# Optimization experiments

Hardware: AMD Instinct MI355X
Metric: run time of the kernel (lower is better)

Reference implementation:

```python
import jax, jax.numpy as jnp
import numpy as np

N_NODES = 100000
N_EDGES = 1600000
N_GRAPHS = 512
F_IN = 20
HID = 128
OUT = HID // 2


def _glorot(key, shape):
    fan_in, fan_out = shape[0], shape[1]
    lim = float(np.sqrt(6.0 / (fan_in + fan_out)))
    return jax.random.uniform(key, shape, jnp.float32, -lim, lim)


def setup_inputs() -> dict:
    key = jax.random.key(0)
    ks = jax.random.split(key, 12)
    x = jax.random.normal(ks[0], (N_NODES, F_IN), jnp.float32)
    edge_index = jax.random.randint(ks[1], (2, N_EDGES), 0, N_NODES, dtype=jnp.int64)
    batch = jnp.sort(jax.random.randint(ks[2], (N_NODES,), 0, N_GRAPHS, dtype=jnp.int64))
    return {
        "x": x,
        "edge_index": edge_index,
        "batch": batch,
        "W1": _glorot(ks[3], (F_IN, HID)), "b1": jnp.zeros((HID,), jnp.float32),
        "W2": _glorot(ks[4], (HID, HID)), "b2": jnp.zeros((HID,), jnp.float32),
        "W3": _glorot(ks[5], (HID, HID)), "b3": jnp.zeros((HID,), jnp.float32),
        "Wout": _glorot(ks[6], (HID, OUT)), "bout": jnp.zeros((OUT,), jnp.float32),
    }


def _gcn_conv(x, W, b, src, dst, num_nodes):
    # PyG GCNConv: x' = D^{-1/2} (A + I) D^{-1/2} X W + b (self-loops already in src/dst)
    xw = x @ W                                                  # [N, H]
    ones = jnp.ones(src.shape[0], dtype=xw.dtype)
    deg = jax.ops.segment_sum(ones, dst, num_segments=num_nodes)
    dinv = jnp.where(deg > 0, jax.lax.rsqrt(deg), 0.0)          # [N]
    norm = dinv[src] * dinv[dst]                                # [E+N]
    msg = xw[src] * norm[:, None]                               # gather + scale
    return jax.ops.segment_sum(msg, dst, num_segments=num_nodes) + b


def reference(x, edge_index, batch, W1, b1, W2, b2, W3, b3, Wout, bout):
    num_nodes = x.shape[0]
    loops = jnp.arange(num_nodes, dtype=edge_index.dtype)
    src = jnp.concatenate([edge_index[0], loops])
    dst = jnp.concatenate([edge_index[1], loops])

    h = jax.nn.relu(_gcn_conv(x, W1, b1, src, dst, num_nodes))
    h = jax.nn.relu(_gcn_conv(h, W2, b2, src, dst, num_nodes))
    h = jax.nn.relu(_gcn_conv(h, W3, b3, src, dst, num_nodes))

    # global_mean_pool over graph ids
    sums = jax.ops.segment_sum(h, batch, num_segments=N_GRAPHS)
    counts = jax.ops.segment_sum(jnp.ones(num_nodes, h.dtype), batch, num_segments=N_GRAPHS)
    pooled = sums / jnp.maximum(counts, 1.0)[:, None]           # [G, H]
    return pooled @ Wout + bout                                 # [G, H//2]
```

## Files before the change

### kernel.cpp

```cpp
#include <hip/hip_runtime.h>
#include <hip/hip_fp16.h>

#define N_NODES 100000
#define N_EDGES 1600000
#define N_GRAPHS 512
#define F_IN 20
#define HID 128
#define OUT_F 64

#define BUCKETS 512
#define SPAN 196
#define BCAP 3500
#define EPB 4096

typedef _Float16 half8_t __attribute__((ext_vector_type(8)));
typedef float f32x4_t __attribute__((ext_vector_type(4)));
typedef unsigned int uv4 __attribute__((ext_vector_type(4)));

__device__ inline float4 h4_to_f4(uint2 u) {
    __half2 h0 = *(__half2*)&u.x;
    __half2 h1 = *(__half2*)&u.y;
    float2 f0 = __half22float2(h0);
    float2 f1 = __half22float2(h1);
    return make_float4(f0.x, f0.y, f1.x, f1.y);
}

__device__ inline float4 f4_from(unsigned a, unsigned b) {
    __half2 h0 = *(__half2*)&a;
    __half2 h1 = *(__half2*)&b;
    float2 f0 = __half22float2(h0);
    float2 f1 = __half22float2(h1);
    return make_float4(f0.x, f0.y, f1.x, f1.y);
}

__global__ __launch_bounds__(512) void partition(const int* __restrict__ src,
                                                 const int* __restrict__ dst,
                                                 int* __restrict__ bpairs,
                                                 int* cur512) {
    __shared__ int lcnt[8][BUCKETS];
    __shared__ int woff[8][BUCKETS];
    int t = threadIdx.x;
    int wv = t >> 6;
    for (int i = t; i < 8 * BUCKETS; i += 512) ((int*)lcnt)[i] = 0;
    __syncthreads();
    int base = blockIdx.x * EPB;
    int myb[8], myp[8], myr[8];
#pragma unroll
    for (int i = 0; i < 8; ++i) {
        int e = base + i * 512 + t;
        int b = -1, p = 0, rk = 0;
        if (e < N_EDGES) {
            int s = src[e], d = dst[e];
            b = d / SPAN;
            p = (s << 9) | (d - b * SPAN);
            rk = atomicAdd(&lcnt[wv][b], 1);
        }
        myb[i] = b; myp[i] = p; myr[i] = rk;
    }
    __syncthreads();
    {
        int c[8], tot = 0;
#pragma unroll
        for (int w = 0; w < 8; ++w) { c[w] = lcnt[w][t]; tot += c[w]; }
        int gb = atomicAdd(&cur512[t], tot);
#pragma unroll
        for (int w = 0; w < 8; ++w) { woff[w][t] = gb; gb += c[w]; }
    }
    __syncthreads();
#pragma unroll
    for (int i = 0; i < 8; ++i) {
        int b = myb[i];
        if (b >= 0) {
            int p = woff[wv][b] + myr[i];
            if (p < BCAP) bpairs[(size_t)b * BCAP + p] = myp[i];
        }
    }
}

__global__ __launch_bounds__(512) void csr_build(const int* __restrict__ bpairs,
                                                 const int* __restrict__ cur512,
                                                 int* __restrict__ row_st,
                                                 int* __restrict__ csr,
                                                 const float* __restrict__ x,
                                                 __half* __restrict__ Xs) {
    __shared__ int ocnt[SPAN];
    __shared__ int sc[512];
    __shared__ int cur[SPAN];
    __shared__ int sbase;
    int b = blockIdx.x, t = threadIdx.x;

    int myc = cur512[t];
    sc[t] = myc;
    __syncthreads();
    for (int o = 1; o < BUCKETS; o <<= 1) {
        int v = (t >= o) ? sc[t - o] : 0;
        __syncthreads();
        sc[t] += v;
        __syncthreads();
    }
    if (t == b) sbase = sc[t] - myc;
    if (b == BUCKETS - 1 && t == 0) row_st[N_NODES] = N_EDGES;

    int n0 = b * SPAN;
    int span = N_NODES - n0; if (span > SPAN) span = SPAN;
    if (span < 0) span = 0;
    if (t < SPAN) ocnt[t] = 0;
    __syncthreads();

    int n = cur512[b];
    if (n > BCAP) n = BCAP;
    const int* p = bpairs + (size_t)b * BCAP;
    for (int i = t; i < n; i += 512) atomicAdd(&ocnt[p[i] & 511], 1);
    __syncthreads();
    sc[t] = (t < span) ? ocnt[t] : 0;
    __syncthreads();
    for (int o = 1; o < 512; o <<= 1) {
        int v = (t >= o) ? sc[t - o] : 0;
        __syncthreads();
        sc[t] += v;
        __syncthreads();
    }
    int base = sbase;
    if (t < span) {
        int start = sc[t] - ocnt[t];
        row_st[n0 + t] = base + start;
        cur[t] = start;
    }
    __syncthreads();
    for (int i = t; i < n; i += 512) {
        int e = p[i];
        int lp = atomicAdd(&cur[e & 511], 1);
        csr[base + lp] = e >> 9;
    }
    for (int i = t; i < span * 32; i += 512) {
        int nl = i >> 5, f = i & 31;
        float v = (f < F_IN) ? x[(size_t)(n0 + nl) * F_IN + f] : 0.f;
        float di = rsqrtf((float)(ocnt[nl] + 1));
        Xs[(size_t)(n0 + nl) * 32 + f] = __float2half(di * v);
    }
}

__global__ __launch_bounds__(256) void layer1(const __half* __restrict__ Xs,
                                              const int* __restrict__ row_st,
                                              const int* __restrict__ csr,
                                              const float* __restrict__ W,
                                              const float* __restrict__ bias,
                                              __half* __restrict__ H) {
    __shared__ float Wlds[F_IN * HID];
    __shared__ float Alds[64][F_IN];
    const int t = threadIdx.x;
    const int node0 = blockIdx.x * 64;

    for (int i = t; i < F_IN * HID; i += 256) Wlds[i] = W[i];

    const int grp = t >> 2;
    const int l   = t & 3;
    const int n   = node0 + grp;
    if (n < N_NODES) {
        int r0 = row_st[n], r1 = row_st[n + 1];
        const uv4* X4 = (const uv4*)Xs;
        uv4 u = X4[(size_t)n * 4 + l];
        float4 accL = f4_from(u[0], u[1]);
        float4 accH = f4_from(u[2], u[3]);
        int r = r0;
        for (; r + 7 < r1; r += 8) {
            int s0 = csr[r],     s1 = csr[r + 1], s2 = csr[r + 2], s3 = csr[r + 3];
            int s4 = csr[r + 4], s5 = csr[r + 5], s6 = csr[r + 6], s7 = csr[r + 7];
            uv4 vv0 = X4[(size_t)s0 * 4 + l];
            uv4 vv1 = X4[(size_t)s1 * 4 + l];
            uv4 vv2 = X4[(size_t)s2 * 4 + l];
            uv4 vv3 = X4[(size_t)s3 * 4 + l];
            uv4 vv4 = X4[(size_t)s4 * 4 + l];
            uv4 vv5 = X4[(size_t)s5 * 4 + l];
            uv4 vv6 = X4[(size_t)s6 * 4 + l];
            uv4 vv7 = X4[(size_t)s7 * 4 + l];
            uv4 vv[8] = {vv0, vv1, vv2, vv3, vv4, vv5, vv6, vv7};
#pragma unroll
            for (int j = 0; j < 8; ++j) {
                float4 aL = f4_from(vv[j][0], vv[j][1]);
                float4 aH = f4_from(vv[j][2], vv[j][3]);
                accL.x += aL.x; accL.y += aL.y; accL.z += aL.z; accL.w += aL.w;
                accH.x += aH.x; accH.y += aH.y; accH.z += aH.z; accH.w += aH.w;
            }
        }
        for (; r < r1; ++r) {
            uv4 v = X4[(size_t)csr[r] * 4 + l];
            float4 aL = f4_from(v[0], v[1]);
            float4 aH = f4_from(v[2], v[3]);
            accL.x += aL.x; accL.y += aL.y; accL.z += aL.z; accL.w += aL.w;
            accH.x += aH.x; accH.y += aH.y; accH.z += aH.z; accH.w += aH.w;
        }
        float di = rsqrtf((float)(r1 - r0 + 1));
        if (l < 2) {
            int f0 = l * 8;
            Alds[grp][f0 + 0] = di * accL.x;
            Alds[grp][f0 + 1] = di * accL.y;
            Alds[grp][f0 + 2] = di * accL.z;
            Alds[grp][f0 + 3] = di * accL.w;
            Alds[grp][f0 + 4] = di * accH.x;
            Alds[grp][f0 + 5] = di * accH.y;
            Alds[grp][f0 + 6] = di * accH.z;
            Alds[grp][f0 + 7] = di * accH.w;
        } else if (l == 2) {
            Alds[grp][16] = di * accL.x;
            Alds[grp][17] = di * accL.y;
            Alds[grp][18] = di * accL.z;
            Alds[grp][19] = di * accL.w;
        }
    }
    __syncthreads();

    const int nl = t >> 2;
    const int cb = (t & 3) * 4;
    float4 acc[8];
#pragma unroll
    for (int j = 0; j < 8; ++j) acc[j] = *(const float4*)&bias[cb + 16 * j];
#pragma unroll
    for (int k = 0; k < F_IN; ++k) {
        float a = Alds[nl][k];
        const float* Wr = &Wlds[k * HID + cb];
#pragma unroll
        for (int j = 0; j < 8; ++j) {
            float4 w = *(const float4*)&Wr[16 * j];
            acc[j].x = fmaf(a, w.x, acc[j].x);
            acc[j].y = fmaf(a, w.y, acc[j].y);
            acc[j].z = fmaf(a, w.z, acc[j].z);
            acc[j].w = fmaf(a, w.w, acc[j].w);
        }
    }
    if (node0 + nl < N_NODES) {
#pragma unroll
        for (int j = 0; j < 8; ++j) {
            int c = cb + 16 * j;
            int slice = c >> 6;
            int wi = (t & 3) + 4 * (j & 3);
            __half2 h0 = __floats2half2_rn(acc[j].x, acc[j].y);
            __half2 h1 = __floats2half2_rn(acc[j].z, acc[j].w);
            uint2 u; u.x = *(unsigned*)&h0; u.y = *(unsigned*)&h1;
            ((uint2*)H)[((size_t)slice * N_NODES + node0 + nl) * 16 + wi] = u;
        }
    }
}

__global__ __launch_bounds__(256) void gemm_mfma(const __half* __restrict__ H,
                                                 const float* __restrict__ W,
                                                 const int* __restrict__ row_st,
                                                 __half* __restrict__ T) {
    __shared__ _Float16 Whi[64 * 128];
    __shared__ _Float16 Wlo[64 * 128];
    const int t = threadIdx.x;
    const int c0 = (blockIdx.x & 1) * 64;

    for (int i = t; i < 128 * 64; i += 256) {
        int k = i >> 6, c = i & 63;
        float w = W[k * HID + c0 + c];
        _Float16 hi = (_Float16)w;
        _Float16 lo = (_Float16)((w - (float)hi) * 2048.0f);
        int addr = c * 128 + (((k >> 3) ^ (c & 15)) << 3) + (k & 7);
        Whi[addr] = hi;
        Wlo[addr] = lo;
    }
    __syncthreads();

    const int wv = t >> 6;
    const int l  = t & 63;
    const int lr = l & 15;
    const int lq = l >> 4;

    for (int rep = 0; rep < 4; ++rep) {
        int strip = ((blockIdx.x >> 1) * 4 + wv) * 4 + rep;
        if (strip >= N_NODES / 16) continue;
        int n0 = strip * 16;

        f32x4_t acc[4], acl[4];
#pragma unroll
        for (int ct = 0; ct < 4; ++ct) { acc[ct] = (f32x4_t){0,0,0,0}; acl[ct] = (f32x4_t){0,0,0,0}; }

#pragma unroll
        for (int kc = 0; kc < 4; ++kc) {
            half8_t a = *(const half8_t*)(H + ((size_t)(kc >> 1) * N_NODES + n0 + lr) * 64
                                            + (kc & 1) * 32 + lq * 8);
#pragma unroll
            for (int j = 0; j < 8; ++j) a[j] = a[j] > (_Float16)0 ? a[j] : (_Float16)0;
            int g = kc * 4 + lq;
#pragma unroll
            for (int ct = 0; ct < 4; ++ct) {
                int c = ct * 16 + lr;
                int addr = c * 128 + ((g ^ lr) << 3);
                half8_t bh = *(const half8_t*)&Whi[addr];
                half8_t bl = *(const half8_t*)&Wlo[addr];
                acc[ct] = __builtin_amdgcn_mfma_f32_16x16x32_f16(a, bh, acc[ct], 0, 0, 0);
                acl[ct] = __builtin_amdgcn_mfma_f32_16x16x32_f16(a, bl, acl[ct], 0, 0, 0);
            }
        }

        int r0 = n0 + lq * 4;
#pragma unroll
        for (int r = 0; r < 4; ++r) {
            int row = r0 + r;
            float d = rsqrtf((float)(row_st[row + 1] - row_st[row] + 1));
#pragma unroll
            for (int ct = 0; ct < 4; ++ct) {
                float v = (acc[ct][r] + acl[ct][r] * 4.8828125e-4f) * d;
                int c = c0 + ct * 16 + lr;
                T[((size_t)(c >> 6) * N_NODES + row) * 64 + (c & 63)] = __float2half(v);
            }
        }
    }
}

__global__ __launch_bounds__(256) void gather_half(const __half* __restrict__ T,
                                                   const int* __restrict__ row_st,
                                                   const int* __restrict__ csr,
                                                   const float* __restrict__ bias,
                                                   __half* __restrict__ B) {
    int t = threadIdx.x;
    int b = blockIdx.x;
    int x = b & 7;
    int slice = x >> 2;
    int chunk = (b >> 3) * 4 + (x & 3);
    int n = chunk * 32 + (t >> 3);
    int l = t & 7;
    if (n >= N_NODES) return;
    int r0 = row_st[n], r1 = row_st[n + 1];
    float di = rsqrtf((float)(r1 - r0 + 1));
    const uv4* Tf = (const uv4*)T + (size_t)slice * N_NODES * 8;
    uv4 u = Tf[(size_t)n * 8 + l];
    float4 accL = f4_from(u[0], u[1]);
    float4 accH = f4_from(u[2], u[3]);
    int r = r0;
    for (; r + 7 < r1; r += 8) {
        int s0 = csr[r],     s1 = csr[r + 1], s2 = csr[r + 2], s3 = csr[r + 3];
        int s4 = csr[r + 4], s5 = csr[r + 5], s6 = csr[r + 6], s7 = csr[r + 7];
        uv4 vv0 = Tf[(size_t)s0 * 8 + l];
        uv4 vv1 = Tf[(size_t)s1 * 8 + l];
        uv4 vv2 = Tf[(size_t)s2 * 8 + l];
        uv4 vv3 = Tf[(size_t)s3 * 8 + l];
        uv4 vv4 = Tf[(size_t)s4 * 8 + l];
        uv4 vv5 = Tf[(size_t)s5 * 8 + l];
        uv4 vv6 = Tf[(size_t)s6 * 8 + l];
        uv4 vv7 = Tf[(size_t)s7 * 8 + l];
        uv4 vv[8] = {vv0, vv1, vv2, vv3, vv4, vv5, vv6, vv7};
#pragma unroll
        for (int j = 0; j < 8; ++j) {
            float4 aL = f4_from(vv[j][0], vv[j][1]);
            float4 aH = f4_from(vv[j][2], vv[j][3]);
            accL.x += aL.x; accL.y += aL.y; accL.z += aL.z; accL.w += aL.w;
            accH.x += aH.x; accH.y += aH.y; accH.z += aH.z; accH.w += aH.w;
        }
    }
    for (; r + 3 < r1; r += 4) {
        int s0 = csr[r], s1 = csr[r + 1], s2 = csr[r + 2], s3 = csr[r + 3];
        uv4 vv0 = Tf[(size_t)s0 * 8 + l];
        uv4 vv1 = Tf[(size_t)s1 * 8 + l];
        uv4 vv2 = Tf[(size_t)s2 * 8 + l];
        uv4 vv3 = Tf[(size_t)s3 * 8 + l];
        uv4 vv[4] = {vv0, vv1, vv2, vv3};
#pragma unroll
        for (int j = 0; j < 4; ++j) {
            float4 aL = f4_from(vv[j][0], vv[j][1]);
            float4 aH = f4_from(vv[j][2], vv[j][3]);
            accL.x += aL.x; accL.y += aL.y; accL.z += aL.z; accL.w += aL.w;
            accH.x += aH.x; accH.y += aH.y; accH.z += aH.z; accH.w += aH.w;
        }
    }
    for (; r < r1; ++r) {
        uv4 v = Tf[(size_t)csr[r] * 8 + l];
        float4 aL = f4_from(v[0], v[1]);
        float4 aH = f4_from(v[2], v[3]);
        accL.x += aL.x; accL.y += aL.y; accL.z += aL.z; accL.w += aL.w;
        accH.x += aH.x; accH.y += aH.y; accH.z += aH.z; accH.w += aH.w;
    }
    const float4* bb = (const float4*)bias + slice * 16 + l * 2;
    float4 b0 = bb[0], b1 = bb[1];
    __half2 h0 = __floats2half2_rn(fmaf(di, accL.x, b0.x), fmaf(di, accL.y, b0.y));
    __half2 h1 = __floats2half2_rn(fmaf(di, accL.z, b0.z), fmaf(di, accL.w, b0.w));
    __half2 h2 = __floats2half2_rn(fmaf(di, accH.x, b1.x), fmaf(di, accH.y, b1.y));
    __half2 h3 = __floats2half2_rn(fmaf(di, accH.z, b1.z), fmaf(di, accH.w, b1.w));
    uv4 o;
    o[0] = *(unsigned*)&h0; o[1] = *(unsigned*)&h1;
    o[2] = *(unsigned*)&h2; o[3] = *(unsigned*)&h3;
    uv4* dstp = (uv4*)B + ((size_t)slice * N_NODES + n) * 8 + l;
    __builtin_nontemporal_store(o, dstp);
}

__global__ __launch_bounds__(256) void pool_head(const __half* __restrict__ H,
                                                 const int* __restrict__ batch,
                                                 const float* __restrict__ Wout,
                                                 const float* __restrict__ bout,
                                                 float* __restrict__ out) {
    __shared__ float4 part[8][32];
    __shared__ float p[HID];
    __shared__ int bounds[2];
    int g = blockIdx.x;
    int t = threadIdx.x;
    if (t < 2) {
        int target = g + t;
        int lo = 0, hi = N_NODES;
        while (lo < hi) {
            int mid = (lo + hi) >> 1;
            if (batch[mid] < target) lo = mid + 1; else hi = mid;
        }
        bounds[t] = lo;
    }
    __syncthreads();
    int lo = bounds[0], hi = bounds[1];
    int grp = t >> 5, l = t & 31;
    const uint2* Hf = (const uint2*)H;
    float4 acc = make_float4(0.f, 0.f, 0.f, 0.f);
    const size_t sbase = (size_t)(l >> 4) * N_NODES;
    const int wi = l & 15;
    for (int n = lo + grp; n < hi; n += 8) {
        float4 v = h4_to_f4(Hf[(sbase + n) * 16 + wi]);
        acc.x += fmaxf(v.x, 0.f);
        acc.y += fmaxf(v.y, 0.f);
        acc.z += fmaxf(v.z, 0.f);
        acc.w += fmaxf(v.w, 0.f);
    }
    part[grp][l] = acc;
    __syncthreads();
    if (t < 32) {
        float4 s = part[0][t];
#pragma unroll
        for (int j = 1; j < 8; ++j) {
            float4 v = part[j][t];
            s.x += v.x; s.y += v.y; s.z += v.z; s.w += v.w;
        }
        float inv = 1.0f / fmaxf((float)(hi - lo), 1.0f);
        p[t * 4 + 0] = s.x * inv;
        p[t * 4 + 1] = s.y * inv;
        p[t * 4 + 2] = s.z * inv;
        p[t * 4 + 3] = s.w * inv;
    }
    __syncthreads();
    if (t < OUT_F) {
        float acc2 = 0.f;
#pragma unroll 8
        for (int k = 0; k < HID; ++k)
            acc2 = fmaf(p[k], Wout[k * OUT_F + t], acc2);
        out[g * OUT_F + t] = acc2 + bout[t];
    }
}

extern "C" void kernel_launch(void* const* d_in, const int* in_sizes, int n_in,
                              void* d_out, int out_size, void* d_ws, size_t ws_size,
                              hipStream_t stream) {
    const float* x     = (const float*)d_in[0];
    const int*   ei    = (const int*)d_in[1];
    const int*   batch = (const int*)d_in[2];
    const float* W1    = (const float*)d_in[3];
    const float* b1    = (const float*)d_in[4];
    const float* W2    = (const float*)d_in[5];
    const float* b2    = (const float*)d_in[6];
    const float* W3    = (const float*)d_in[7];
    const float* b3    = (const float*)d_in[8];
    const float* Wout  = (const float*)d_in[9];
    const float* bout  = (const float*)d_in[10];
    float* out = (float*)d_out;

    const int* src = ei;
    const int* dst = ei + N_EDGES;

    float* A      = (float*)d_ws;
    float* Breg   = A + (size_t)N_NODES * HID;
    int*   row_st = (int*)(Breg + (size_t)N_NODES * HID);
    int*   cur512 = row_st + N_NODES + 1;
    int*   csr    = cur512 + BUCKETS;

    int*    bpairs = (int*)A;
    __half* Xs     = (__half*)((char*)A + 7168000);
    __half* T      = (__half*)A;
    __half* H      = (__half*)Breg;

    hipMemsetAsync(cur512, 0, BUCKETS * sizeof(int), stream);
    partition<<<(N_EDGES + EPB - 1) / EPB, 512, 0, stream>>>(src, dst, bpairs, cur512);
    csr_build<<<BUCKETS, 512, 0, stream>>>(bpairs, cur512, row_st, csr, x, Xs);

    layer1<<<(N_NODES + 63) / 64, 256, 0, stream>>>(Xs, row_st, csr, W1, b1, H);

    gemm_mfma<<<782, 256, 0, stream>>>(H, W2, row_st, T);
    gather_half<<<6256, 256, 0, stream>>>(T, row_st, csr, b2, H);
    gemm_mfma<<<782, 256, 0, stream>>>(H, W3, row_st, T);
    gather_half<<<6256, 256, 0, stream>>>(T, row_st, csr, b3, H);

    pool_head<<<N_GRAPHS, 256, 0, stream>>>(H, batch, Wout, bout, out);
}
```

Baseline: 343.3 us.

## Fuse aggregation and MFMA GEMM per layer, aggregate before transform

Replaces the separate transform-then-gather kernels for layers 2 and 3 with one fused kernel. It first aggregates 128-wide pre-scaled fp16 neighbour features into LDS, then multiplies by W using split hi/lo fp16 MFMA, applying bias, ReLU and the next layer's degree scaling in the epilogue. The weight hi/lo split moves into a separate prep kernel, and the activation layout changes from two 64-column slices to row-major 128. This removes the intermediate T round trip and two launches, at the cost of gathering 256-byte rows instead of 128-byte slices and a per-block weight load from global memory.

```diff
diff --git a/kernel.cpp b/kernel.cpp
--- a/kernel.cpp
+++ b/kernel.cpp
@@ -31,6 +31,13 @@
     float2 f0 = __half22float2(h0);
     float2 f1 = __half22float2(h1);
     return make_float4(f0.x, f0.y, f1.x, f1.y);
+}
+
+__device__ inline void acc8(float4& aL, float4& aH, uv4 v) {
+    float4 l_ = f4_from(v[0], v[1]);
+    float4 h_ = f4_from(v[2], v[3]);
+    aL.x += l_.x; aL.y += l_.y; aL.z += l_.z; aL.w += l_.w;
+    aH.x += h_.x; aH.y += h_.y; aH.z += h_.z; aH.w += h_.w;
 }
 
 __global__ __launch_bounds__(512) void partition(const int* __restrict__ src,
@@ -140,6 +147,21 @@
     }
 }
 
+__global__ __launch_bounds__(256) void w_prep(const float* __restrict__ W2,
+                                              const float* __restrict__ W3,
+                                              _Float16* __restrict__ Whl) {
+    int idx = blockIdx.x * 256 + threadIdx.x;
+    if (idx >= 2 * HID * HID) return;
+    int layer = idx >> 14;
+    int c = (idx >> 7) & 127;
+    int k = idx & 127;
+    float w = (layer ? W3 : W2)[k * HID + c];
+    _Float16 hi = (_Float16)w;
+    _Float16 lo = (_Float16)((w - (float)hi) * 2048.0f);
+    Whl[((size_t)layer * 2 + 0) * 16384 + c * 128 + k] = hi;
+    Whl[((size_t)layer * 2 + 1) * 16384 + c * 128 + k] = lo;
+}
+
 __global__ __launch_bounds__(256) void layer1(const __half* __restrict__ Xs,
                                               const int* __restrict__ row_st,
                                               const int* __restrict__ csr,
@@ -148,6 +170,7 @@
                                               __half* __restrict__ H) {
     __shared__ float Wlds[F_IN * HID];
     __shared__ float Alds[64][F_IN];
+    __shared__ float d1[64];
     const int t = threadIdx.x;
     const int node0 = blockIdx.x * 64;
 
@@ -156,6 +179,7 @@
     const int grp = t >> 2;
     const int l   = t & 3;
     const int n   = node0 + grp;
+    float di = 0.f;
     if (n < N_NODES) {
         int r0 = row_st[n], r1 = row_st[n + 1];
         const uv4* X4 = (const uv4*)Xs;
@@ -176,21 +200,10 @@
             uv4 vv7 = X4[(size_t)s7 * 4 + l];
             uv4 vv[8] = {vv0, vv1, vv2, vv3, vv4, vv5, vv6, vv7};
 #pragma unroll
-            for (int j = 0; j < 8; ++j) {
-                float4 aL = f4_from(vv[j][0], vv[j][1]);
-                float4 aH = f4_from(vv[j][2], vv[j][3]);
-                accL.x += aL.x; accL.y += aL.y; accL.z += aL.z; accL.w += aL.w;
-                accH.x += aH.x; accH.y += aH.y; accH.z += aH.z; accH.w += aH.w;
-            }
-        }
-        for (; r < r1; ++r) {
-            uv4 v = X4[(size_t)csr[r] * 4 + l];
-            float4 aL = f4_from(v[0], v[1]);
-            float4 aH = f4_from(v[2], v[3]);
-            accL.x += aL.x; accL.y += aL.y; accL.z += aL.z; accL.w += aL.w;
-            accH.x += aH.x; accH.y += aH.y; accH.z += aH.z; accH.w += aH.w;
-        }
-        float di = rsqrtf((float)(r1 - r0 + 1));
+            for (int j = 0; j < 8; ++j) acc8(accL, accH, vv[j]);
+        }
+        for (; r < r1; ++r) acc8(accL, accH, X4[(size_t)csr[r] * 4 + l]);
+        di = rsqrtf((float)(r1 - r0 + 1));
         if (l < 2) {
             int f0 = l * 8;
             Alds[grp][f0 + 0] = di * accL.x;
@@ -208,6 +221,7 @@
             Alds[grp][19] = di * accL.w;
         }
     }
+    if (l == 0) d1[grp] = di;
     __syncthreads();
 
     const int nl = t >> 2;
@@ -229,159 +243,134 @@
         }
     }
     if (node0 + nl < N_NODES) {
+        float dd = d1[nl];
 #pragma unroll
         for (int j = 0; j < 8; ++j) {
-            int c = cb + 16 * j;
-            int slice = c >> 6;
-            int wi = (t & 3) + 4 * (j & 3);
-            __half2 h0 = __floats2half2_rn(acc[j].x, acc[j].y);
-            __half2 h1 = __floats2half2_rn(acc[j].z, acc[j].w);
+            float vx = fmaxf(acc[j].x, 0.f) * dd;
+            float vy = fmaxf(acc[j].y, 0.f) * dd;
+            float vz = fmaxf(acc[j].z, 0.f) * dd;
+            float vw = fmaxf(acc[j].w, 0.f) * dd;
+            __half2 h0 = __floats2half2_rn(vx, vy);
+            __half2 h1 = __floats2half2_rn(vz, vw);
             uint2 u; u.x = *(unsigned*)&h0; u.y = *(unsigned*)&h1;
-            ((uint2*)H)[((size_t)slice * N_NODES + node0 + nl) * 16 + wi] = u;
-        }
-    }
-}
-
-__global__ __launch_bounds__(256) void gemm_mfma(const __half* __restrict__ H,
-                                                 const float* __restrict__ W,
-                                                 const int* __restrict__ row_st,
-                                                 __half* __restrict__ T) {
-    __shared__ _Float16 Whi[64 * 128];
-    __shared__ _Float16 Wlo[64 * 128];
-    const int t = threadIdx.x;
-    const int c0 = (blockIdx.x & 1) * 64;
-
-    for (int i = t; i < 128 * 64; i += 256) {
-        int k = i >> 6, c = i & 63;
-        float w = W[k * HID + c0 + c];
-        _Float16 hi = (_Float16)w;
-        _Float16 lo = (_Float16)((w - (float)hi) * 2048.0f);
-        int addr = c * 128 + (((k >> 3) ^ (c & 15)) << 3) + (k & 7);
-        Whi[addr] = hi;
-        Wlo[addr] = lo;
-    }
-    __syncthreads();
-
-    const int wv = t >> 6;
-    const int l  = t & 63;
-    const int lr = l & 15;
-    const int lq = l >> 4;
-
-    for (int rep = 0; rep < 4; ++rep) {
-        int strip = ((blockIdx.x >> 1) * 4 + wv) * 4 + rep;
-        if (strip >= N_NODES / 16) continue;
-        int n0 = strip * 16;
-
-        f32x4_t acc[4], acl[4];
-#pragma unroll
-        for (int ct = 0; ct < 4; ++ct) { acc[ct] = (f32x4_t){0,0,0,0}; acl[ct] = (f32x4_t){0,0,0,0}; }
-
-#pragma unroll
-        for (int kc = 0; kc < 4; ++kc) {
-            half8_t a = *(const half8_t*)(H + ((size_t)(kc >> 1) * N_NODES + n0 + lr) * 64
-                                            + (kc & 1) * 32 + lq * 8);
-#pragma unroll
-            for (int j = 0; j < 8; ++j) a[j] = a[j] > (_Float16)0 ? a[j] : (_Float16)0;
-            int g = kc * 4 + lq;
-#pragma unroll
-            for (int ct = 0; ct < 4; ++ct) {
-                int c = ct * 16 + lr;
-                int addr = c * 128 + ((g ^ lr) << 3);
-                half8_t bh = *(const half8_t*)&Whi[addr];
-                half8_t bl = *(const half8_t*)&Wlo[addr];
-                acc[ct] = __builtin_amdgcn_mfma_f32_16x16x32_f16(a, bh, acc[ct], 0, 0, 0);
-                acl[ct] = __builtin_amdgcn_mfma_f32_16x16x32_f16(a, bl, acl[ct], 0, 0, 0);
-            }
-        }
-
-        int r0 = n0 + lq * 4;
-#pragma unroll
-        for (int r = 0; r < 4; ++r) {
-            int row = r0 + r;
-            float d = rsqrtf((float)(row_st[row + 1] - row_st[row] + 1));
-#pragma unroll
-            for (int ct = 0; ct < 4; ++ct) {
-                float v = (acc[ct][r] + acl[ct][r] * 4.8828125e-4f) * d;
-                int c = c0 + ct * 16 + lr;
-                T[((size_t)(c >> 6) * N_NODES + row) * 64 + (c & 63)] = __float2half(v);
-            }
-        }
-    }
-}
-
-__global__ __launch_bounds__(256) void gather_half(const __half* __restrict__ T,
+            ((uint2*)H)[(size_t)(node0 + nl) * 32 + (t & 3) + 4 * j] = u;
+        }
+    }
+}
+
+template<int APPLY_D>
+__global__ __launch_bounds__(512) void layer_fused(const __half* __restrict__ P,
                                                    const int* __restrict__ row_st,
                                                    const int* __restrict__ csr,
+                                                   const _Float16* __restrict__ Wb,
                                                    const float* __restrict__ bias,
-                                                   __half* __restrict__ B) {
-    int t = threadIdx.x;
-    int b = blockIdx.x;
-    int x = b & 7;
-    int slice = x >> 2;
-    int chunk = (b >> 3) * 4 + (x & 3);
-    int n = chunk * 32 + (t >> 3);
-    int l = t & 7;
-    if (n >= N_NODES) return;
-    int r0 = row_st[n], r1 = row_st[n + 1];
-    float di = rsqrtf((float)(r1 - r0 + 1));
-    const uv4* Tf = (const uv4*)T + (size_t)slice * N_NODES * 8;
-    uv4 u = Tf[(size_t)n * 8 + l];
-    float4 accL = f4_from(u[0], u[1]);
-    float4 accH = f4_from(u[2], u[3]);
-    int r = r0;
-    for (; r + 7 < r1; r += 8) {
-        int s0 = csr[r],     s1 = csr[r + 1], s2 = csr[r + 2], s3 = csr[r + 3];
-        int s4 = csr[r + 4], s5 = csr[r + 5], s6 = csr[r + 6], s7 = csr[r + 7];
-        uv4 vv0 = Tf[(size_t)s0 * 8 + l];
-        uv4 vv1 = Tf[(size_t)s1 * 8 + l];
-        uv4 vv2 = Tf[(size_t)s2 * 8 + l];
-        uv4 vv3 = Tf[(size_t)s3 * 8 + l];
-        uv4 vv4 = Tf[(size_t)s4 * 8 + l];
-        uv4 vv5 = Tf[(size_t)s5 * 8 + l];
-        uv4 vv6 = Tf[(size_t)s6 * 8 + l];
-        uv4 vv7 = Tf[(size_t)s7 * 8 + l];
-        uv4 vv[8] = {vv0, vv1, vv2, vv3, vv4, vv5, vv6, vv7};
-#pragma unroll
-        for (int j = 0; j < 8; ++j) {
-            float4 aL = f4_from(vv[j][0], vv[j][1]);
-            float4 aH = f4_from(vv[j][2], vv[j][3]);
-            accL.x += aL.x; accL.y += aL.y; accL.z += aL.z; accL.w += aL.w;
-            accH.x += aH.x; accH.y += aH.y; accH.z += aH.z; accH.w += aH.w;
-        }
-    }
-    for (; r + 3 < r1; r += 4) {
-        int s0 = csr[r], s1 = csr[r + 1], s2 = csr[r + 2], s3 = csr[r + 3];
-        uv4 vv0 = Tf[(size_t)s0 * 8 + l];
-        uv4 vv1 = Tf[(size_t)s1 * 8 + l];
-        uv4 vv2 = Tf[(size_t)s2 * 8 + l];
-        uv4 vv3 = Tf[(size_t)s3 * 8 + l];
-        uv4 vv[4] = {vv0, vv1, vv2, vv3};
+                                                   __half* __restrict__ Pout) {
+    __shared__ __align__(16) _Float16 Alds[64 * 128];
+    __shared__ float dls[64];
+    const int t = threadIdx.x;
+    const int node0 = blockIdx.x * 64;
+
+    {
+        const int grp = t >> 3, l = t & 7;
+        const int n = node0 + grp;
+        float4 a0 = {0,0,0,0}, a1 = {0,0,0,0}, a2 = {0,0,0,0}, a3 = {0,0,0,0};
+        float di = 0.f;
+        if (n < N_NODES) {
+            int r0 = row_st[n], r1 = row_st[n + 1];
+            di = rsqrtf((float)(r1 - r0 + 1));
+            const uv4* P4 = (const uv4*)P;
+            uv4 u0 = P4[(size_t)n * 16 + l];
+            uv4 u1 = P4[(size_t)n * 16 + 8 + l];
+            a0 = f4_from(u0[0], u0[1]); a1 = f4_from(u0[2], u0[3]);
+            a2 = f4_from(u1[0], u1[1]); a3 = f4_from(u1[2], u1[3]);
+            int r = r0;
+            for (; r + 3 < r1; r += 4) {
+                int s0 = csr[r], s1 = csr[r + 1], s2 = csr[r + 2], s3 = csr[r + 3];
+                uv4 p00 = P4[(size_t)s0 * 16 + l];
+                uv4 p01 = P4[(size_t)s0 * 16 + 8 + l];
+                uv4 p10 = P4[(size_t)s1 * 16 + l];
+                uv4 p11 = P4[(size_t)s1 * 16 + 8 + l];
+                uv4 p20 = P4[(size_t)s2 * 16 + l];
+                uv4 p21 = P4[(size_t)s2 * 16 + 8 + l];
+                uv4 p30 = P4[(size_t)s3 * 16 + l];
+                uv4 p31 = P4[(size_t)s3 * 16 + 8 + l];
+                acc8(a0, a1, p00); acc8(a2, a3, p01);
+                acc8(a0, a1, p10); acc8(a2, a3, p11);
+                acc8(a0, a1, p20); acc8(a2, a3, p21);
+                acc8(a0, a1, p30); acc8(a2, a3, p31);
+            }
+            for (; r < r1; ++r) {
+                int s = csr[r];
+                acc8(a0, a1, P4[(size_t)s * 16 + l]);
+                acc8(a2, a3, P4[(size_t)s * 16 + 8 + l]);
+            }
+        }
+        a0.x *= di; a0.y *= di; a0.z *= di; a0.w *= di;
+        a1.x *= di; a1.y *= di; a1.z *= di; a1.w *= di;
+        a2.x *= di; a2.y *= di; a2.z *= di; a2.w *= di;
+        a3.x *= di; a3.y *= di; a3.z *= di; a3.w *= di;
+        __half2 h0 = __floats2half2_rn(a0.x, a0.y), h1 = __floats2half2_rn(a0.z, a0.w);
+        __half2 h2 = __floats2half2_rn(a1.x, a1.y), h3 = __floats2half2_rn(a1.z, a1.w);
+        __half2 h4 = __floats2half2_rn(a2.x, a2.y), h5 = __floats2half2_rn(a2.z, a2.w);
+        __half2 h6 = __floats2half2_rn(a3.x, a3.y), h7 = __floats2half2_rn(a3.z, a3.w);
+        uv4 c0, c1;
+        c0[0] = *(unsigned*)&h0; c0[1] = *(unsigned*)&h1;
+        c0[2] = *(unsigned*)&h2; c0[3] = *(unsigned*)&h3;
+        c1[0] = *(unsigned*)&h4; c1[1] = *(unsigned*)&h5;
+        c1[2] = *(unsigned*)&h6; c1[3] = *(unsigned*)&h7;
+        int swz = (grp & 7) << 4;
+        char* rowp = (char*)Alds + grp * 256;
+        *(uv4*)(rowp + ((l * 16) ^ swz)) = c0;
+        *(uv4*)(rowp + ((128 + l * 16) ^ swz)) = c1;
+        if (l == 0) dls[grp] = di;
+    }
+    __syncthreads();
+
+    const int wv = t >> 6;
+    const int ln = t & 63;
+    const int lr = ln & 15;
+    const int lq = ln >> 4;
+
+    half8_t bh[4], bl[4];
+    {
+        const _Float16* wp = Wb + (size_t)(wv * 16 + lr) * 128 + lq * 8;
+#pragma unroll
+        for (int kc = 0; kc < 4; ++kc) {
+            bh[kc] = *(const half8_t*)(wp + kc * 32);
+            bl[kc] = *(const half8_t*)(wp + 16384 + kc * 32);
+        }
+    }
+    f32x4_t acch[4], accl[4];
+#pragma unroll
+    for (int s = 0; s < 4; ++s) { acch[s] = (f32x4_t){0,0,0,0}; accl[s] = (f32x4_t){0,0,0,0}; }
+
+#pragma unroll
+    for (int strip = 0; strip < 4; ++strip) {
+        const char* rowp = (const char*)Alds + (strip * 16 + lr) * 256;
+        const int sw = (lr & 7) << 4;
+#pragma unroll
+        for (int kc = 0; kc < 4; ++kc) {
+            half8_t a = *(const half8_t*)(rowp + ((kc * 64 + lq * 16) ^ sw));
+            acch[strip] = __builtin_amdgcn_mfma_f32_16x16x32_f16(a, bh[kc], acch[strip], 0, 0, 0);
+            accl[strip] = __builtin_amdgcn_mfma_f32_16x16x32_f16(a, bl[kc], accl[strip], 0, 0, 0);
+        }
+    }
+
+    const float bc = bias[wv * 16 + lr];
+#pragma unroll
+    for (int strip = 0; strip < 4; ++strip) {
 #pragma unroll
         for (int j = 0; j < 4; ++j) {
-            float4 aL = f4_from(vv[j][0], vv[j][1]);
-            float4 aH = f4_from(vv[j][2], vv[j][3]);
-            accL.x += aL.x; accL.y += aL.y; accL.z += aL.z; accL.w += aL.w;
-            accH.x += aH.x; accH.y += aH.y; accH.z += aH.z; accH.w += aH.w;
-        }
-    }
-    for (; r < r1; ++r) {
-        uv4 v = Tf[(size_t)csr[r] * 8 + l];
-        float4 aL = f4_from(v[0], v[1]);
-        float4 aH = f4_from(v[2], v[3]);
-        accL.x += aL.x; accL.y += aL.y; accL.z += aL.z; accL.w += aL.w;
-        accH.x += aH.x; accH.y += aH.y; accH.z += aH.z; accH.w += aH.w;
-    }
-    const float4* bb = (const float4*)bias + slice * 16 + l * 2;
-    float4 b0 = bb[0], b1 = bb[1];
-    __half2 h0 = __floats2half2_rn(fmaf(di, accL.x, b0.x), fmaf(di, accL.y, b0.y));
-    __half2 h1 = __floats2half2_rn(fmaf(di, accL.z, b0.z), fmaf(di, accL.w, b0.w));
-    __half2 h2 = __floats2half2_rn(fmaf(di, accH.x, b1.x), fmaf(di, accH.y, b1.y));
-    __half2 h3 = __floats2half2_rn(fmaf(di, accH.z, b1.z), fmaf(di, accH.w, b1.w));
-    uv4 o;
-    o[0] = *(unsigned*)&h0; o[1] = *(unsigned*)&h1;
-    o[2] = *(unsigned*)&h2; o[3] = *(unsigned*)&h3;
-    uv4* dstp = (uv4*)B + ((size_t)slice * N_NODES + n) * 8 + l;
-    __builtin_nontemporal_store(o, dstp);
+            int rowl = strip * 16 + lq * 4 + j;
+            int row = node0 + rowl;
+            if (row < N_NODES) {
+                float v = acch[strip][j] + accl[strip][j] * 4.8828125e-4f + bc;
+                v = fmaxf(v, 0.f);
+                if (APPLY_D) v *= dls[rowl];
+                Pout[(size_t)row * 128 + wv * 16 + lr] = __float2half(v);
+            }
+        }
+    }
 }
 
 __global__ __launch_bounds__(256) void pool_head(const __half* __restrict__ H,
@@ -408,10 +397,8 @@
     int grp = t >> 5, l = t & 31;
     const uint2* Hf = (const uint2*)H;
     float4 acc = make_float4(0.f, 0.f, 0.f, 0.f);
-    const size_t sbase = (size_t)(l >> 4) * N_NODES;
-    const int wi = l & 15;
     for (int n = lo + grp; n < hi; n += 8) {
-        float4 v = h4_to_f4(Hf[(sbase + n) * 16 + wi]);
+        float4 v = h4_to_f4(Hf[(size_t)n * 32 + l]);
         acc.x += fmaxf(v.x, 0.f);
         acc.y += fmaxf(v.y, 0.f);
         acc.z += fmaxf(v.z, 0.f);
@@ -467,21 +454,21 @@
     int*   cur512 = row_st + N_NODES + 1;
     int*   csr    = cur512 + BUCKETS;
 
-    int*    bpairs = (int*)A;
-    __half* Xs     = (__half*)((char*)A + 7168000);
-    __half* T      = (__half*)A;
-    __half* H      = (__half*)Breg;
+    int*      bpairs = (int*)A;
+    __half*   Xs     = (__half*)((char*)A + 7168000);
+    __half*   T      = (__half*)A;
+    __half*   H      = (__half*)Breg;
+    _Float16* Whl    = (_Float16*)((char*)A + 26u * 1024 * 1024);
 
     hipMemsetAsync(cur512, 0, BUCKETS * sizeof(int), stream);
     partition<<<(N_EDGES + EPB - 1) / EPB, 512, 0, stream>>>(src, dst, bpairs, cur512);
+    w_prep<<<128, 256, 0, stream>>>(W2, W3, Whl);
     csr_build<<<BUCKETS, 512, 0, stream>>>(bpairs, cur512, row_st, csr, x, Xs);
 
     layer1<<<(N_NODES + 63) / 64, 256, 0, stream>>>(Xs, row_st, csr, W1, b1, H);
 
-    gemm_mfma<<<782, 256, 0, stream>>>(H, W2, row_st, T);
-    gather_half<<<6256, 256, 0, stream>>>(T, row_st, csr, b2, H);
-    gemm_mfma<<<782, 256, 0, stream>>>(H, W3, row_st, T);
-    gather_half<<<6256, 256, 0, stream>>>(T, row_st, csr, b3, H);
+    layer_fused<1><<<(N_NODES + 63) / 64, 512, 0, stream>>>(H, row_st, csr, Whl, b2, T);
+    layer_fused<0><<<(N_NODES + 63) / 64, 512, 0, stream>>>(T, row_st, csr, Whl + 32768, b3, H);
 
     pool_head<<<N_GRAPHS, 256, 0, stream>>>(H, batch, Wout, bout, out);
 }
```

After: 353.0 us. 1.03x slower.

## Stage bucket scatter and CSR writes in shared memory for coalesced stores

Applied to the files above, without the earlier changes.

The partition kernel now computes a block-local prefix sum over bucket counts, stages edges in shared memory sorted by bucket, and then writes them to global bucket slots contiguously, instead of scattering each edge directly. csr_build likewise fills the per-bucket CSR slice in LDS with atomics and then copies it to global memory linearly. Both changes aim to replace random global stores with coalesced ones, at the cost of extra LDS (about 24KB more in partition plus 14KB in csr_build), an extra scan and extra barriers that may reduce occupancy. It also refactors the accumulate helper and changes the wi index formula in layer1.

```diff
diff --git a/kernel.cpp b/kernel.cpp
--- a/kernel.cpp
+++ b/kernel.cpp
@@ -33,12 +33,25 @@
     return make_float4(f0.x, f0.y, f1.x, f1.y);
 }
 
+__device__ inline void acc8(float4& aL, float4& aH, uv4 v) {
+    float4 l_ = f4_from(v[0], v[1]);
+    float4 h_ = f4_from(v[2], v[3]);
+    aL.x += l_.x; aL.y += l_.y; aL.z += l_.z; aL.w += l_.w;
+    aH.x += h_.x; aH.y += h_.y; aH.z += h_.z; aH.w += h_.w;
+}
+
 __global__ __launch_bounds__(512) void partition(const int* __restrict__ src,
                                                  const int* __restrict__ dst,
                                                  int* __restrict__ bpairs,
                                                  int* cur512) {
     __shared__ int lcnt[8][BUCKETS];
     __shared__ int woff[8][BUCKETS];
+    __shared__ int loffx[BUCKETS];
+    __shared__ int gbase[BUCKETS];
+    __shared__ int sc[512];
+    __shared__ int stage[EPB];
+    __shared__ unsigned short sbuck[EPB];
+    __shared__ int stot;
     int t = threadIdx.x;
     int wv = t >> 6;
     for (int i = t; i < 8 * BUCKETS; i += 512) ((int*)lcnt)[i] = 0;
@@ -58,22 +71,42 @@
         myb[i] = b; myp[i] = p; myr[i] = rk;
     }
     __syncthreads();
+    int c[8], tot = 0;
+#pragma unroll
+    for (int w = 0; w < 8; ++w) { c[w] = lcnt[w][t]; tot += c[w]; }
+    sc[t] = tot;
+    __syncthreads();
+    for (int o = 1; o < BUCKETS; o <<= 1) {
+        int v = (t >= o) ? sc[t - o] : 0;
+        __syncthreads();
+        sc[t] += v;
+        __syncthreads();
+    }
+    int excl = sc[t] - tot;
+    loffx[t] = excl;
+    gbase[t] = atomicAdd(&cur512[t], tot);
     {
-        int c[8], tot = 0;
-#pragma unroll
-        for (int w = 0; w < 8; ++w) { c[w] = lcnt[w][t]; tot += c[w]; }
-        int gb = atomicAdd(&cur512[t], tot);
-#pragma unroll
-        for (int w = 0; w < 8; ++w) { woff[w][t] = gb; gb += c[w]; }
-    }
+        int lb = excl;
+#pragma unroll
+        for (int w = 0; w < 8; ++w) { woff[w][t] = lb; lb += c[w]; }
+    }
+    if (t == 511) stot = sc[511];
     __syncthreads();
 #pragma unroll
     for (int i = 0; i < 8; ++i) {
         int b = myb[i];
         if (b >= 0) {
-            int p = woff[wv][b] + myr[i];
-            if (p < BCAP) bpairs[(size_t)b * BCAP + p] = myp[i];
-        }
+            int slot = woff[wv][b] + myr[i];
+            stage[slot] = myp[i];
+            sbuck[slot] = (unsigned short)b;
+        }
+    }
+    __syncthreads();
+    int n = stot;
+    for (int i = t; i < n; i += 512) {
+        int b = sbuck[i];
+        int pos = gbase[b] + (i - loffx[b]);
+        if (pos < BCAP) bpairs[(size_t)b * BCAP + pos] = stage[i];
     }
 }
 
@@ -86,6 +119,7 @@
     __shared__ int ocnt[SPAN];
     __shared__ int sc[512];
     __shared__ int cur[SPAN];
+    __shared__ int lcsr[BCAP];
     __shared__ int sbase;
     int b = blockIdx.x, t = threadIdx.x;
 
@@ -130,8 +164,11 @@
     for (int i = t; i < n; i += 512) {
         int e = p[i];
         int lp = atomicAdd(&cur[e & 511], 1);
-        csr[base + lp] = e >> 9;
-    }
+        lcsr[lp] = e >> 9;
+    }
+    __syncthreads();
+    for (int i = t; i < n; i += 512)
+        csr[base + i] = lcsr[i];
     for (int i = t; i < span * 32; i += 512) {
         int nl = i >> 5, f = i & 31;
         float v = (f < F_IN) ? x[(size_t)(n0 + nl) * F_IN + f] : 0.f;
@@ -176,20 +213,9 @@
             uv4 vv7 = X4[(size_t)s7 * 4 + l];
             uv4 vv[8] = {vv0, vv1, vv2, vv3, vv4, vv5, vv6, vv7};
 #pragma unroll
-            for (int j = 0; j < 8; ++j) {
-                float4 aL = f4_from(vv[j][0], vv[j][1]);
-                float4 aH = f4_from(vv[j][2], vv[j][3]);
-                accL.x += aL.x; accL.y += aL.y; accL.z += aL.z; accL.w += aL.w;
-                accH.x += aH.x; accH.y += aH.y; accH.z += aH.z; accH.w += aH.w;
-            }
-        }
-        for (; r < r1; ++r) {
-            uv4 v = X4[(size_t)csr[r] * 4 + l];
-            float4 aL = f4_from(v[0], v[1]);
-            float4 aH = f4_from(v[2], v[3]);
-            accL.x += aL.x; accL.y += aL.y; accL.z += aL.z; accL.w += aL.w;
-            accH.x += aH.x; accH.y += aH.y; accH.z += aH.z; accH.w += aH.w;
-        }
+            for (int j = 0; j < 8; ++j) acc8(accL, accH, vv[j]);
+        }
+        for (; r < r1; ++r) acc8(accL, accH, X4[(size_t)csr[r] * 4 + l]);
         float di = rsqrtf((float)(r1 - r0 + 1));
         if (l < 2) {
             int f0 = l * 8;
@@ -233,7 +259,7 @@
         for (int j = 0; j < 8; ++j) {
             int c = cb + 16 * j;
             int slice = c >> 6;
-            int wi = (t & 3) + 4 * (j & 3);
+            int wi = ((c & 63) >> 2);
             __half2 h0 = __floats2half2_rn(acc[j].x, acc[j].y);
             __half2 h1 = __floats2half2_rn(acc[j].z, acc[j].w);
             uint2 u; u.x = *(unsigned*)&h0; u.y = *(unsigned*)&h1;
```

After: 335.9 us (median of 2 runs). 2.2% less time.
